# Performance work log

Hardware: AMD Instinct MI355X
Metric: run time of the kernel (lower is better)

Reference implementation:

```python
import jax, jax.numpy as jnp
import numpy as np

N = 1_000_000      # neurons (scaled-up NEURON_COUNT)
E = 20_000_000     # synapses (scaled-up NEURON_COUNT * SYNAPSE_RATIO)
IN = 4096          # input_size
OUT = 4096         # output_size
STEPS = 3


def setup_inputs() -> dict:
    key = jax.random.key(0)
    k1, k2, k3, k4, k5 = jax.random.split(key, 5)
    x = jax.random.normal(k1, (IN,), jnp.float32)
    synapse_src = jax.random.randint(k2, (E,), 0, N)
    synapse_dst = jax.random.randint(k3, (E,), 0, N)
    synapse_weights = jax.random.normal(k4, (E,), jnp.float32)
    neuron_biases = jax.random.normal(k5, (N - IN,), jnp.float32)
    input_indices = jnp.arange(IN)              # first IN neurons are inputs
    output_indices = jnp.arange(N - OUT, N)     # last OUT neurons are outputs
    non_input_indices = jnp.arange(IN, N)       # complement of input_indices
    return {
        "x": x,
        "synapse_weights": synapse_weights,
        "neuron_biases": neuron_biases,
        "synapse_src": synapse_src,
        "synapse_dst": synapse_dst,
        "input_indices": input_indices,
        "output_indices": output_indices,
        "non_input_indices": non_input_indices,
    }


def reference(x, synapse_weights, neuron_biases, synapse_src, synapse_dst,
              input_indices, output_indices, non_input_indices):
    # out_mask[i] True => neuron i is an output (skipped by tanh)
    out_mask = jnp.zeros(N, dtype=bool).at[output_indices].set(True)
    # initial state: zeros with inputs written in
    v = jnp.zeros(N, dtype=x.dtype).at[input_indices].set(x)
    for _ in range(STEPS):
        # per-edge multiply + scatter-add into destination neurons
        msgs = v[synapse_src] * synapse_weights          # [E]
        nxt = jax.ops.segment_sum(msgs, synapse_dst, num_segments=N)  # [N]
        # bias only for non-input neurons
        nxt = nxt.at[non_input_indices].add(neuron_biases)
        # tanh everywhere except output neurons
        v = jnp.where(out_mask, nxt, jnp.tanh(nxt))
    return v[output_indices]
```

## Files before the change

### kernel.cpp

```cpp
#include <hip/hip_runtime.h>

#define THREADS 256
#define BTHREADS 1024
#define SCTHREADS 1024
#define BSHIFT 12
#define BSIZE 4096
#define NBMAX 256
#define SC_CHUNK 32768
#define PASS_EDGES 8192
#define EPT 8
typedef unsigned int u32;
typedef unsigned long long u64;


__global__ void prep_kernel(const float* __restrict__ x, const float* __restrict__ bias,
                            float* __restrict__ v, float* __restrict__ nxt,
                            int N, int IN) {
    int i = blockIdx.x * THREADS + threadIdx.x;
    if (i >= N) return;
    v[i]   = (i < IN) ? x[i] : 0.0f;
    nxt[i] = (i < IN) ? 0.0f : bias[i - IN];
}

__global__ void edge0_kernel(const int* __restrict__ src, const int* __restrict__ dst,
                             const float* __restrict__ w, const float* __restrict__ v,
                             float* __restrict__ nxt, int E, int IN) {
    int k = blockIdx.x * THREADS + threadIdx.x;
    int E4 = E >> 2;
    if (k < E4) {
        int4 s = ((const int4*)src)[k];
        int b = k << 2;
        if (s.x < IN) atomicAdd(&nxt[dst[b + 0]], v[s.x] * w[b + 0]);
        if (s.y < IN) atomicAdd(&nxt[dst[b + 1]], v[s.y] * w[b + 1]);
        if (s.z < IN) atomicAdd(&nxt[dst[b + 2]], v[s.z] * w[b + 2]);
        if (s.w < IN) atomicAdd(&nxt[dst[b + 3]], v[s.w] * w[b + 3]);
    }
    if (k == 0) {
        for (int e = E4 << 2; e < E; ++e) {
            int s = src[e];
            if (s < IN) atomicAdd(&nxt[dst[e]], v[s] * w[e]);
        }
    }
}

__global__ void finalize0_kernel(float* __restrict__ v, int N, int OUT) {
    int i = blockIdx.x * THREADS + threadIdx.x;
    if (i >= N) return;
    float val = v[i];
    v[i] = (i >= N - OUT) ? val : tanhf(val);
}

__global__ void histo_kernel(const int* __restrict__ dst, u32* __restrict__ ghisto,
                             int E) {
    __shared__ u32 h[NBMAX];
    for (int i = threadIdx.x; i < NBMAX; i += THREADS) h[i] = 0;
    __syncthreads();
    int stride = gridDim.x * THREADS;
    for (int e = blockIdx.x * THREADS + threadIdx.x; e < E; e += stride)
        atomicAdd(&h[((u32)dst[e]) >> BSHIFT], 1u);
    __syncthreads();
    for (int i = threadIdx.x; i < NBMAX; i += THREADS) {
        u32 c = h[i];
        if (c) atomicAdd(&ghisto[i], c);
    }
}

__global__ void scan_kernel(const u32* __restrict__ ghisto, u32* __restrict__ gbase,
                            u32* __restrict__ gcursor, int NB) {
    __shared__ u32 s[NBMAX];
    int t = threadIdx.x;
    u32 own = (t < NB) ? ghisto[t] : 0u;
    s[t] = own;
    __syncthreads();
    for (int off = 1; off < NBMAX; off <<= 1) {
        u32 v = (t >= off) ? s[t - off] : 0u;
        __syncthreads();
        s[t] += v;
        __syncthreads();
    }
    u32 excl = s[t] - own;
    if (t < NB) { gbase[t] = excl; gcursor[t] = excl; }
    if (t == NB - 1) gbase[NB] = s[t];
}

__global__ void __launch_bounds__(SCTHREADS)
scatter_kernel(const int* __restrict__ src, const int* __restrict__ dst,
               const float* __restrict__ w, u32* __restrict__ gcursor,
               uint2* __restrict__ e8, int E) {
    __shared__ uint2 stage[PASS_EDGES];
    __shared__ u32 hc[NBMAX];
    __shared__ u32 runStart[NBMAX + 1];
    __shared__ u32 gpos[NBMAX];
    __shared__ u32 sc[NBMAX];

    const int tid = threadIdx.x;
    int blockStart = blockIdx.x * SC_CHUNK;
    int blockEnd = blockStart + SC_CHUNK; if (blockEnd > E) blockEnd = E;

    for (int ps = blockStart; ps < blockEnd; ps += PASS_EDGES) {
        int base = ps + tid * EPT;
        u32 pk[EPT]; u32 bk[EPT]; u32 wb[EPT];
        int cnt = 0;
        if (base + EPT <= blockEnd) {
            int4 s0 = *(const int4*)(src + base), s1 = *(const int4*)(src + base + 4);
            int4 d0 = *(const int4*)(dst + base), d1 = *(const int4*)(dst + base + 4);
            float4 w0 = *(const float4*)(w + base), w1 = *(const float4*)(w + base + 4);
            int ss[EPT] = {s0.x, s0.y, s0.z, s0.w, s1.x, s1.y, s1.z, s1.w};
            int dd[EPT] = {d0.x, d0.y, d0.z, d0.w, d1.x, d1.y, d1.z, d1.w};
            float ww[EPT] = {w0.x, w0.y, w0.z, w0.w, w1.x, w1.y, w1.z, w1.w};
            cnt = EPT;
            #pragma unroll
            for (int i = 0; i < EPT; ++i) {
                u32 d = (u32)dd[i];
                bk[i] = d >> BSHIFT;
                pk[i] = (u32)ss[i] | ((d & (BSIZE - 1u)) << 20);
                wb[i] = __float_as_uint(ww[i]);
            }
        } else {
            for (int i = 0; i < EPT; ++i) {
                int e = base + i;
                if (e < blockEnd) {
                    u32 d = (u32)dst[e];
                    bk[cnt] = d >> BSHIFT;
                    pk[cnt] = (u32)src[e] | ((d & (BSIZE - 1u)) << 20);
                    wb[cnt] = __float_as_uint(w[e]);
                    ++cnt;
                }
            }
        }
        if (tid < NBMAX) hc[tid] = 0;
        __syncthreads();
        for (int i = 0; i < cnt; ++i) atomicAdd(&hc[bk[i]], 1u);
        __syncthreads();
        u32 own = (tid < NBMAX) ? hc[tid] : 0u;
        if (tid < NBMAX) sc[tid] = own;
        __syncthreads();
        for (int off = 1; off < NBMAX; off <<= 1) {
            u32 t = 0;
            if (tid < NBMAX && tid >= off) t = sc[tid - off];
            __syncthreads();
            if (tid < NBMAX) sc[tid] += t;
            __syncthreads();
        }
        if (tid < NBMAX) {
            runStart[tid] = sc[tid] - own;
            gpos[tid] = own ? atomicAdd(&gcursor[tid], own) : 0u;
            hc[tid] = 0;
        }
        if (tid == NBMAX - 1) runStart[NBMAX] = sc[tid];
        __syncthreads();
        for (int i = 0; i < cnt; ++i) {
            u32 r = atomicAdd(&hc[bk[i]], 1u);
            stage[runStart[bk[i]] + r] = make_uint2(pk[i], wb[i]);
        }
        __syncthreads();
        int wave = tid >> 6, lane = tid & 63;
        for (int b = wave; b < NBMAX; b += (SCTHREADS >> 6)) {
            u32 s0 = runStart[b], s1 = runStart[b + 1], gp = gpos[b];
            for (u32 j = s0 + lane; j < s1; j += 64)
                e8[gp + (j - s0)] = stage[j];
        }
        __syncthreads();
    }
}

__global__ void __launch_bounds__(BTHREADS)
bucket_step_kernel(const uint2* __restrict__ e8,
                   const u32* __restrict__ gbase,
                   const float* __restrict__ v_in,
                   float* __restrict__ v_out,
                   const float* __restrict__ bias,
                   float* __restrict__ out,
                   int N, int IN, int OUT) {
    __shared__ float acc[BSIZE];
    for (int i = threadIdx.x; i < BSIZE; i += BTHREADS) acc[i] = 0.0f;
    __syncthreads();
    int b = blockIdx.x;
    u32 beg = gbase[b], end = gbase[b + 1];
    for (u32 e = beg + threadIdx.x; e < end; e += BTHREADS) {
        u64 pv = __builtin_nontemporal_load((const u64*)(e8 + e));
        u32 px = (u32)pv;
        float pw = __uint_as_float((u32)(pv >> 32));
        u32 s = px & 0xFFFFFu;
        u32 dl = px >> 20;
        atomicAdd(&acc[dl], v_in[s] * pw);
    }
    __syncthreads();
    int base = b << BSHIFT;
    for (int j = threadIdx.x; j < BSIZE; j += BTHREADS) {
        int idx = base + j;
        if (idx >= N) break;
        float val = acc[j] + (idx >= IN ? bias[idx - IN] : 0.0f);
        bool isOut = idx >= N - OUT;
        float a = isOut ? val : tanhf(val);
        v_out[idx] = a;
        if (out != nullptr && isOut) out[idx - (N - OUT)] = a;
    }
}


__global__ void edge_kernel(const int* __restrict__ src, const int* __restrict__ dst,
                            const float* __restrict__ w, const float* __restrict__ v,
                            float* __restrict__ nxt, int E) {
    int k = blockIdx.x * THREADS + threadIdx.x;
    int E4 = E >> 2;
    if (k < E4) {
        int4 s = ((const int4*)src)[k];
        int4 d = ((const int4*)dst)[k];
        float4 wv = ((const float4*)w)[k];
        atomicAdd(&nxt[d.x], v[s.x] * wv.x);
        atomicAdd(&nxt[d.y], v[s.y] * wv.y);
        atomicAdd(&nxt[d.z], v[s.z] * wv.z);
        atomicAdd(&nxt[d.w], v[s.w] * wv.w);
    }
    if (k == 0) {
        for (int e = E4 << 2; e < E; ++e)
            atomicAdd(&nxt[dst[e]], v[src[e]] * w[e]);
    }
}

__global__ void finalize_kernel(float* __restrict__ nxt, float* __restrict__ v,
                                const float* __restrict__ bias, float* __restrict__ out,
                                int N, int IN, int OUT) {
    int i = blockIdx.x * THREADS + threadIdx.x;
    if (i >= N) return;
    float val = nxt[i];
    bool isOut = (i >= N - OUT);
    float a = isOut ? val : tanhf(val);
    v[i] = a;
    nxt[i] = (i < IN) ? 0.0f : bias[i - IN];
    if (out != nullptr && isOut) out[i - (N - OUT)] = a;
}


extern "C" void kernel_launch(void* const* d_in, const int* in_sizes, int n_in,
                              void* d_out, int out_size, void* d_ws, size_t ws_size,
                              hipStream_t stream) {
    const float* x    = (const float*)d_in[0];
    const float* w    = (const float*)d_in[1];
    const float* bias = (const float*)d_in[2];
    const int* src = (const int*)d_in[3];
    const int* dst = (const int*)d_in[4];

    const int IN  = in_sizes[0];
    const int E   = in_sizes[1];
    const int N   = IN + in_sizes[2];
    const int OUT = out_size;

    uint2* e8     = (uint2*)d_ws;
    u32*   ghisto = (u32*)(e8 + E);
    u32*   gbase  = ghisto + NBMAX;
    u32*   gcursor= gbase + NBMAX + 1;
    float* vA     = (float*)(gcursor + NBMAX);
    float* vB     = vA + N;
    size_t need   = (size_t)((char*)(vB + N) - (char*)d_ws);

    int nBlocks = (N + THREADS - 1) / THREADS;
    int eBlocks = ((E >> 2) + THREADS - 1) / THREADS;

    if (ws_size >= need && N <= (1 << 20)) {
        int NB = (N + BSIZE - 1) >> BSHIFT;
        hipMemsetAsync(ghisto, 0, NBMAX * sizeof(u32), stream);
        prep_kernel<<<nBlocks, THREADS, 0, stream>>>(x, bias, vA, vB, N, IN);
        histo_kernel<<<1024, THREADS, 0, stream>>>(dst, ghisto, E);
        scan_kernel<<<1, NBMAX, 0, stream>>>(ghisto, gbase, gcursor, NB);
        scatter_kernel<<<(E + SC_CHUNK - 1) / SC_CHUNK, SCTHREADS, 0, stream>>>(
            src, dst, w, gcursor, e8, E);
        edge0_kernel<<<eBlocks, THREADS, 0, stream>>>(src, dst, w, vA, vB, E, IN);
        finalize0_kernel<<<nBlocks, THREADS, 0, stream>>>(vB, N, OUT);
        bucket_step_kernel<<<NB, BTHREADS, 0, stream>>>(
            e8, gbase, vB, vA, bias, nullptr, N, IN, OUT);
        bucket_step_kernel<<<NB, BTHREADS, 0, stream>>>(
            e8, gbase, vA, vB, bias, (float*)d_out, N, IN, OUT);
    } else {
        float* v   = (float*)d_ws;
        float* nxt = v + N;
        prep_kernel<<<nBlocks, THREADS, 0, stream>>>(x, bias, v, nxt, N, IN);
        for (int step = 0; step < 3; ++step) {
            edge_kernel<<<eBlocks, THREADS, 0, stream>>>(src, dst, w, v, nxt, E);
            float* outp = (step == 2) ? (float*)d_out : nullptr;
            finalize_kernel<<<nBlocks, THREADS, 0, stream>>>(nxt, v, bias, outp, N, IN, OUT);
        }
    }
}
```

Baseline: 711.1 us.

## Replace global bucket sort with per-pass local sort plus bucket directory

Removes the global histogram and scan kernels. Each 8192-edge pass is now sorted locally by destination bucket and written contiguously, and a u16 directory records where each bucket's run starts within each pass. The step-0 input-edge atomics are folded into the scatter pass, and buckets are halved to 2048 neurons so there are more blocks. The bucket step kernel then walks about 2442 short runs per bucket with 16-lane subgroups, which gives up long coalesced streams and adds directory reads in exchange for dropping two launches and a full pass over dst.

```diff
diff --git a/kernel.cpp b/kernel.cpp
--- a/kernel.cpp
+++ b/kernel.cpp
@@ -3,13 +3,14 @@
 #define THREADS 256
 #define BTHREADS 1024
 #define SCTHREADS 1024
-#define BSHIFT 12
-#define BSIZE 4096
-#define NBMAX 256
-#define SC_CHUNK 32768
+#define BSHIFT 11
+#define BSIZE 2048
+#define NBMAX 512
 #define PASS_EDGES 8192
 #define EPT 8
+#define NPMAX 2560
 typedef unsigned int u32;
+typedef unsigned short u16;
 typedef unsigned long long u64;
 
 
@@ -22,27 +23,6 @@
     nxt[i] = (i < IN) ? 0.0f : bias[i - IN];
 }
 
-__global__ void edge0_kernel(const int* __restrict__ src, const int* __restrict__ dst,
-                             const float* __restrict__ w, const float* __restrict__ v,
-                             float* __restrict__ nxt, int E, int IN) {
-    int k = blockIdx.x * THREADS + threadIdx.x;
-    int E4 = E >> 2;
-    if (k < E4) {
-        int4 s = ((const int4*)src)[k];
-        int b = k << 2;
-        if (s.x < IN) atomicAdd(&nxt[dst[b + 0]], v[s.x] * w[b + 0]);
-        if (s.y < IN) atomicAdd(&nxt[dst[b + 1]], v[s.y] * w[b + 1]);
-        if (s.z < IN) atomicAdd(&nxt[dst[b + 2]], v[s.z] * w[b + 2]);
-        if (s.w < IN) atomicAdd(&nxt[dst[b + 3]], v[s.w] * w[b + 3]);
-    }
-    if (k == 0) {
-        for (int e = E4 << 2; e < E; ++e) {
-            int s = src[e];
-            if (s < IN) atomicAdd(&nxt[dst[e]], v[s] * w[e]);
-        }
-    }
-}
-
 __global__ void finalize0_kernel(float* __restrict__ v, int N, int OUT) {
     int i = blockIdx.x * THREADS + threadIdx.x;
     if (i >= N) return;
@@ -50,58 +30,30 @@
     v[i] = (i >= N - OUT) ? val : tanhf(val);
 }
 
-__global__ void histo_kernel(const int* __restrict__ dst, u32* __restrict__ ghisto,
-                             int E) {
-    __shared__ u32 h[NBMAX];
-    for (int i = threadIdx.x; i < NBMAX; i += THREADS) h[i] = 0;
-    __syncthreads();
-    int stride = gridDim.x * THREADS;
-    for (int e = blockIdx.x * THREADS + threadIdx.x; e < E; e += stride)
-        atomicAdd(&h[((u32)dst[e]) >> BSHIFT], 1u);
-    __syncthreads();
-    for (int i = threadIdx.x; i < NBMAX; i += THREADS) {
-        u32 c = h[i];
-        if (c) atomicAdd(&ghisto[i], c);
-    }
-}
-
-__global__ void scan_kernel(const u32* __restrict__ ghisto, u32* __restrict__ gbase,
-                            u32* __restrict__ gcursor, int NB) {
-    __shared__ u32 s[NBMAX];
-    int t = threadIdx.x;
-    u32 own = (t < NB) ? ghisto[t] : 0u;
-    s[t] = own;
-    __syncthreads();
-    for (int off = 1; off < NBMAX; off <<= 1) {
-        u32 v = (t >= off) ? s[t - off] : 0u;
-        __syncthreads();
-        s[t] += v;
-        __syncthreads();
-    }
-    u32 excl = s[t] - own;
-    if (t < NB) { gbase[t] = excl; gcursor[t] = excl; }
-    if (t == NB - 1) gbase[NB] = s[t];
-}
-
 __global__ void __launch_bounds__(SCTHREADS)
 scatter_kernel(const int* __restrict__ src, const int* __restrict__ dst,
-               const float* __restrict__ w, u32* __restrict__ gcursor,
-               uint2* __restrict__ e8, int E) {
+               const float* __restrict__ w,
+               const float* __restrict__ vA,
+               float* __restrict__ vB,
+               uint2* __restrict__ e8, u16* __restrict__ dir,
+               int E, int IN, int NB, int NP) {
     __shared__ uint2 stage[PASS_EDGES];
     __shared__ u32 hc[NBMAX];
     __shared__ u32 runStart[NBMAX + 1];
-    __shared__ u32 gpos[NBMAX];
-    __shared__ u32 sc[NBMAX];
 
     const int tid = threadIdx.x;
-    int blockStart = blockIdx.x * SC_CHUNK;
-    int blockEnd = blockStart + SC_CHUNK; if (blockEnd > E) blockEnd = E;
-
-    for (int ps = blockStart; ps < blockEnd; ps += PASS_EDGES) {
+    for (int i = tid; i < NBMAX; i += SCTHREADS) hc[i] = 0;
+    __syncthreads();
+
+    for (int p = blockIdx.x; p < NP; p += gridDim.x) {
+        int ps = p * PASS_EDGES;
+        int pe = ps + PASS_EDGES; if (pe > E) pe = E;
+        int cntAll = pe - ps;
+
         int base = ps + tid * EPT;
         u32 pk[EPT]; u32 bk[EPT]; u32 wb[EPT];
         int cnt = 0;
-        if (base + EPT <= blockEnd) {
+        if (base + EPT <= pe) {
             int4 s0 = *(const int4*)(src + base), s1 = *(const int4*)(src + base + 4);
             int4 d0 = *(const int4*)(dst + base), d1 = *(const int4*)(dst + base + 4);
             float4 w0 = *(const float4*)(w + base), w1 = *(const float4*)(w + base + 4);
@@ -115,80 +67,99 @@
                 bk[i] = d >> BSHIFT;
                 pk[i] = (u32)ss[i] | ((d & (BSIZE - 1u)) << 20);
                 wb[i] = __float_as_uint(ww[i]);
+                if (ss[i] < IN) atomicAdd(&vB[dd[i]], vA[ss[i]] * ww[i]);
             }
         } else {
             for (int i = 0; i < EPT; ++i) {
                 int e = base + i;
-                if (e < blockEnd) {
+                if (e < pe) {
+                    int s = src[e];
                     u32 d = (u32)dst[e];
+                    float wv = w[e];
                     bk[cnt] = d >> BSHIFT;
-                    pk[cnt] = (u32)src[e] | ((d & (BSIZE - 1u)) << 20);
-                    wb[cnt] = __float_as_uint(w[e]);
+                    pk[cnt] = (u32)s | ((d & (BSIZE - 1u)) << 20);
+                    wb[cnt] = __float_as_uint(wv);
+                    if (s < IN) atomicAdd(&vB[d], vA[s] * wv);
                     ++cnt;
                 }
             }
         }
+
+        for (int i = 0; i < cnt; ++i) atomicAdd(&hc[bk[i]], 1u);
+        __syncthreads();
+
+        if (tid < 64) {
+            u32 c[8]; u32 s = 0;
+            #pragma unroll
+            for (int k = 0; k < 8; ++k) { c[k] = hc[tid * 8 + k]; s += c[k]; }
+            u32 inc = s;
+            #pragma unroll
+            for (int off = 1; off < 64; off <<= 1) {
+                u32 t = __shfl_up(inc, off, 64);
+                if (tid >= off) inc += t;
+            }
+            u32 excl = inc - s;
+            #pragma unroll
+            for (int k = 0; k < 8; ++k) {
+                runStart[tid * 8 + k] = excl;
+                excl += c[k];
+                hc[tid * 8 + k] = 0;
+            }
+            if (tid == 63) runStart[NBMAX] = excl;
+        }
+        __syncthreads();
+
+        for (int i = 0; i < cnt; ++i) {
+            u32 b = bk[i];
+            u32 r = atomicAdd(&hc[b], 1u);
+            stage[runStart[b] + r] = make_uint2(pk[i], wb[i]);
+        }
+        __syncthreads();
+
+        for (int j = tid * 2; j + 1 < cntAll; j += SCTHREADS * 2)
+            *(uint4*)(e8 + ps + j) = *(const uint4*)(stage + j);
+        if ((cntAll & 1) && tid == 0) e8[ps + cntAll - 1] = stage[cntAll - 1];
+        if (tid <= NB) dir[(u32)p * (u32)(NB + 1) + tid] = (u16)runStart[tid];
         if (tid < NBMAX) hc[tid] = 0;
         __syncthreads();
-        for (int i = 0; i < cnt; ++i) atomicAdd(&hc[bk[i]], 1u);
-        __syncthreads();
-        u32 own = (tid < NBMAX) ? hc[tid] : 0u;
-        if (tid < NBMAX) sc[tid] = own;
-        __syncthreads();
-        for (int off = 1; off < NBMAX; off <<= 1) {
-            u32 t = 0;
-            if (tid < NBMAX && tid >= off) t = sc[tid - off];
-            __syncthreads();
-            if (tid < NBMAX) sc[tid] += t;
-            __syncthreads();
-        }
-        if (tid < NBMAX) {
-            runStart[tid] = sc[tid] - own;
-            gpos[tid] = own ? atomicAdd(&gcursor[tid], own) : 0u;
-            hc[tid] = 0;
-        }
-        if (tid == NBMAX - 1) runStart[NBMAX] = sc[tid];
-        __syncthreads();
-        for (int i = 0; i < cnt; ++i) {
-            u32 r = atomicAdd(&hc[bk[i]], 1u);
-            stage[runStart[bk[i]] + r] = make_uint2(pk[i], wb[i]);
-        }
-        __syncthreads();
-        int wave = tid >> 6, lane = tid & 63;
-        for (int b = wave; b < NBMAX; b += (SCTHREADS >> 6)) {
-            u32 s0 = runStart[b], s1 = runStart[b + 1], gp = gpos[b];
-            for (u32 j = s0 + lane; j < s1; j += 64)
-                e8[gp + (j - s0)] = stage[j];
-        }
-        __syncthreads();
     }
 }
 
 __global__ void __launch_bounds__(BTHREADS)
-bucket_step_kernel(const uint2* __restrict__ e8,
-                   const u32* __restrict__ gbase,
-                   const float* __restrict__ v_in,
-                   float* __restrict__ v_out,
+bucket_step_kernel(const uint2* __restrict__ e8, const u16* __restrict__ dir,
+                   const float* __restrict__ v_in, float* __restrict__ v_out,
                    const float* __restrict__ bias,
                    float* __restrict__ out,
-                   int N, int IN, int OUT) {
+                   int N, int IN, int OUT, int NB, int NP) {
     __shared__ float acc[BSIZE];
-    for (int i = threadIdx.x; i < BSIZE; i += BTHREADS) acc[i] = 0.0f;
+    __shared__ u16 rs[NPMAX], re[NPMAX];
+    const int tid = threadIdx.x;
+    const int b = blockIdx.x;
+
+    for (int p = tid; p < NP; p += BTHREADS) {
+        const u16* row = dir + (u32)p * (u32)(NB + 1) + b;
+        rs[p] = row[0];
+        re[p] = row[1];
+    }
+    for (int i = tid; i < BSIZE; i += BTHREADS) acc[i] = 0.0f;
     __syncthreads();
-    int b = blockIdx.x;
-    u32 beg = gbase[b], end = gbase[b + 1];
-    for (u32 e = beg + threadIdx.x; e < end; e += BTHREADS) {
-        u64 pv = __builtin_nontemporal_load((const u64*)(e8 + e));
-        u32 px = (u32)pv;
-        float pw = __uint_as_float((u32)(pv >> 32));
-        u32 s = px & 0xFFFFFu;
-        u32 dl = px >> 20;
-        atomicAdd(&acc[dl], v_in[s] * pw);
+
+    const int sg = tid >> 4, ln = tid & 15;
+    for (int p = sg; p < NP; p += BTHREADS >> 4) {
+        int s0 = rs[p], s1 = re[p];
+        int base = p * PASS_EDGES;
+        for (int j = s0 + ln; j < s1; j += 16) {
+            u64 pv = __builtin_nontemporal_load((const u64*)(e8 + base + j));
+            u32 px = (u32)pv;
+            float pw = __uint_as_float((u32)(pv >> 32));
+            atomicAdd(&acc[px >> 20], v_in[px & 0xFFFFFu] * pw);
+        }
     }
     __syncthreads();
-    int base = b << BSHIFT;
-    for (int j = threadIdx.x; j < BSIZE; j += BTHREADS) {
-        int idx = base + j;
+
+    int nbase = b << BSHIFT;
+    for (int j = tid; j < BSIZE; j += BTHREADS) {
+        int idx = nbase + j;
         if (idx >= N) break;
         float val = acc[j] + (idx >= IN ? bias[idx - IN] : 0.0f);
         bool isOut = idx >= N - OUT;
@@ -247,34 +218,31 @@
     const int N   = IN + in_sizes[2];
     const int OUT = out_size;
 
-    uint2* e8     = (uint2*)d_ws;
-    u32*   ghisto = (u32*)(e8 + E);
-    u32*   gbase  = ghisto + NBMAX;
-    u32*   gcursor= gbase + NBMAX + 1;
-    float* vA     = (float*)(gcursor + NBMAX);
-    float* vB     = vA + N;
-    size_t need   = (size_t)((char*)(vB + N) - (char*)d_ws);
+    const int NP = (E + PASS_EDGES - 1) / PASS_EDGES;
+    const int NB = (N + BSIZE - 1) >> BSHIFT;
+
+    uint2* e8   = (uint2*)d_ws;
+    u16*   dir  = (u16*)(e8 + E);
+    size_t dirB = (size_t)NP * (size_t)(NB + 1) * sizeof(u16);
+    float* vA   = (float*)((char*)dir + ((dirB + 15) & ~(size_t)15));
+    float* vB   = vA + N;
+    size_t need = (size_t)((char*)(vB + N) - (char*)d_ws);
 
     int nBlocks = (N + THREADS - 1) / THREADS;
-    int eBlocks = ((E >> 2) + THREADS - 1) / THREADS;
-
-    if (ws_size >= need && N <= (1 << 20)) {
-        int NB = (N + BSIZE - 1) >> BSHIFT;
-        hipMemsetAsync(ghisto, 0, NBMAX * sizeof(u32), stream);
+
+    if (ws_size >= need && N <= (NBMAX << BSHIFT) && NP <= NPMAX) {
         prep_kernel<<<nBlocks, THREADS, 0, stream>>>(x, bias, vA, vB, N, IN);
-        histo_kernel<<<1024, THREADS, 0, stream>>>(dst, ghisto, E);
-        scan_kernel<<<1, NBMAX, 0, stream>>>(ghisto, gbase, gcursor, NB);
-        scatter_kernel<<<(E + SC_CHUNK - 1) / SC_CHUNK, SCTHREADS, 0, stream>>>(
-            src, dst, w, gcursor, e8, E);
-        edge0_kernel<<<eBlocks, THREADS, 0, stream>>>(src, dst, w, vA, vB, E, IN);
+        scatter_kernel<<<512, SCTHREADS, 0, stream>>>(
+            src, dst, w, vA, vB, e8, dir, E, IN, NB, NP);
         finalize0_kernel<<<nBlocks, THREADS, 0, stream>>>(vB, N, OUT);
         bucket_step_kernel<<<NB, BTHREADS, 0, stream>>>(
-            e8, gbase, vB, vA, bias, nullptr, N, IN, OUT);
+            e8, dir, vB, vA, bias, nullptr, N, IN, OUT, NB, NP);
         bucket_step_kernel<<<NB, BTHREADS, 0, stream>>>(
-            e8, gbase, vA, vB, bias, (float*)d_out, N, IN, OUT);
+            e8, dir, vA, vB, bias, (float*)d_out, N, IN, OUT, NB, NP);
     } else {
         float* v   = (float*)d_ws;
         float* nxt = v + N;
+        int eBlocks = ((E >> 2) + THREADS - 1) / THREADS;
         prep_kernel<<<nBlocks, THREADS, 0, stream>>>(x, bias, v, nxt, N, IN);
         for (int step = 0; step < 3; ++step) {
             edge_kernel<<<eBlocks, THREADS, 0, stream>>>(src, dst, w, v, nxt, E);
```

Result: faster. 668.1 us (-6.0%).
